# Optimization experiments

Hardware: AMD Instinct MI355X
Metric: run time of the kernel (lower is better)

## Reference

```python
import jax, jax.numpy as jnp
import numpy as np

IMG_H, IMG_W = 900, 1600
NUM_CLASSES = 10
NUM_CAMS = 6

# pcdet boxes_to_corners_3d corner template (unit box, centered)
CORNER_TEMPLATE = jnp.array(
    [[1, 1, -1], [1, -1, -1], [-1, -1, -1], [-1, 1, -1],
     [1, 1, 1], [1, -1, 1], [-1, -1, 1], [-1, 1, 1]], dtype=jnp.float32) * 0.5


def boxes_to_corners_3d(boxes):
    # boxes: [N,7] = (x,y,z,dx,dy,dz,heading) -> [N,8,3]
    dims = boxes[:, 3:6]
    corners = dims[:, None, :] * CORNER_TEMPLATE  # [N,8,3]
    yaw = boxes[:, 6]
    c, s = jnp.cos(yaw), jnp.sin(yaw)
    z = jnp.zeros_like(c)
    o = jnp.ones_like(c)
    # rotate_points_along_z: points @ [[c,s,0],[-s,c,0],[0,0,1]]
    rot = jnp.stack([c, s, z, -s, c, z, z, z, o], axis=-1).reshape(-1, 3, 3)
    corners = jnp.einsum('nkj,njm->nkm', corners, rot)
    return corners + boxes[:, None, 0:3]


def box_iou(a, b):
    # a: [M,4], b: [K,4] xyxy -> [M,K]
    lt = jnp.maximum(a[:, None, :2], b[None, :, :2])
    rb = jnp.minimum(a[:, None, 2:], b[None, :, 2:])
    wh = jnp.clip(rb - lt, 0.0)
    inter = wh[..., 0] * wh[..., 1]
    area_a = (a[:, 2] - a[:, 0]) * (a[:, 3] - a[:, 1])
    area_b = (b[:, 2] - b[:, 0]) * (b[:, 3] - b[:, 1])
    union = area_a[:, None] + area_b[None, :] - inter
    return jnp.where(union > 0, inter / union, 0.0)


def _project_boxes(pred_boxes, img_aug_matrix, lidar_aug_matrix, lidar2image):
    # batch index 0 (B=1); returns proj [6,N,4] and valid [6,N]
    N = pred_boxes.shape[0]
    corners = boxes_to_corners_3d(pred_boxes).reshape(-1, 3)  # [N*8,3]
    la = lidar_aug_matrix[0]
    pts = corners - la[:3, 3]
    pts = jnp.linalg.inv(la[:3, :3]) @ pts.T  # [3, N*8]
    l2i = lidar2image[0]
    cc = l2i[:, :3, :3] @ pts + l2i[:, :3, 3][:, :, None]  # [6,3,N*8]
    zc = jnp.clip(cc[:, 2, :], 1e-5, 1e5)
    xy = cc[:, :2, :] / zc[:, None, :]
    cc = jnp.concatenate([xy, zc[:, None, :]], axis=1)
    ia = img_aug_matrix[0]
    cc = ia[:, :3, :3] @ cc + ia[:, :3, 3][:, :, None]
    pix = jnp.transpose(cc[:, :2, :], (0, 2, 1))  # [6, N*8, 2]
    # .long() truncation (non-differentiable in original)
    pix = jax.lax.stop_gradient(pix).astype(jnp.int32)
    px = jnp.clip(pix[..., 0], 0, IMG_W)
    py = jnp.clip(pix[..., 1], 0, IMG_H)
    pix = jnp.stack([px, py], -1).reshape(NUM_CAMS, N, 8, 2).astype(pred_boxes.dtype)
    xy1 = pix.min(axis=2)  # [6,N,2]
    xy2 = pix.max(axis=2)
    valid = jnp.all((xy2 - xy1) > 0, axis=-1)  # [6,N]
    proj = jnp.concatenate([xy1, xy2], axis=-1)  # [6,N,4]
    return proj, valid


def setup_inputs() -> dict:
    rng = np.random.default_rng(0)
    N, M = 4096, 6144
    xy = rng.uniform(-40, 40, (N, 2))
    zc = rng.uniform(-1, 1, (N, 1))
    dims = rng.uniform(1.0, 4.0, (N, 3))
    yaw = rng.uniform(0, 2 * np.pi, (N, 1))
    pred_boxes = np.concatenate([xy, zc, dims, yaw], axis=1).astype(np.float32)
    # 6 cameras: pinhole intrinsics + yaw-spaced extrinsics
    K = np.array([[1000., 0., 800.], [0., 1000., 450.], [0., 0., 1.]])
    l2i = np.zeros((1, NUM_CAMS, 4, 4), np.float32)
    for ci, ang in enumerate(np.linspace(0, 2 * np.pi, NUM_CAMS, endpoint=False)):
        fwd = np.array([np.cos(ang), np.sin(ang), 0.])
        right = np.array([np.sin(ang), -np.cos(ang), 0.])
        down = np.array([0., 0., -1.])
        R = np.stack([right, down, fwd], 0)
        l2i[0, ci, :3, :3] = K @ R
        l2i[0, ci, 3, 3] = 1.0
    img_aug_matrix = np.tile(np.eye(4, dtype=np.float32), (1, NUM_CAMS, 1, 1))
    lidar_aug_matrix = np.eye(4, dtype=np.float32)[None]
    cx = rng.uniform(0, IMG_W, M)
    cy = rng.uniform(0, IMG_H, M)
    w = rng.uniform(20, 300, M)
    h = rng.uniform(20, 300, M)
    det_boxes = np.stack([np.clip(cx - w / 2, 0, IMG_W), np.clip(cy - h / 2, 0, IMG_H),
                          np.clip(cx + w / 2, 0, IMG_W), np.clip(cy + h / 2, 0, IMG_H)], 1).astype(np.float32)
    det_labels = rng.integers(1, NUM_CLASSES + 1, M).astype(np.int32)
    det_scores = rng.uniform(0.05, 1.0, M).astype(np.float32)
    det_batch_idx = np.zeros(M, np.int32)
    det_cam_idx = (np.arange(M) % NUM_CAMS).astype(np.int32)
    return {
        'pred_boxes': jnp.asarray(pred_boxes),
        'img_aug_matrix': jnp.asarray(img_aug_matrix),
        'lidar_aug_matrix': jnp.asarray(lidar_aug_matrix),
        'lidar2image': jnp.asarray(l2i),
        'det_boxes': jnp.asarray(det_boxes),
        'det_labels': jnp.asarray(det_labels),
        'det_scores': jnp.asarray(det_scores),
        'det_batch_idx': jnp.asarray(det_batch_idx),
        'det_cam_idx': jnp.asarray(det_cam_idx),
    }


def reference(pred_boxes, img_aug_matrix, lidar_aug_matrix, lidar2image,
              det_boxes, det_labels, det_scores, det_batch_idx, det_cam_idx):
    proj, valid = _project_boxes(pred_boxes, img_aug_matrix, lidar_aug_matrix, lidar2image)
    label_matrix = jax.nn.one_hot(det_labels - 1, NUM_CLASSES, dtype=det_scores.dtype) * det_scores[:, None]
    probs_sum = jnp.zeros((pred_boxes.shape[0], NUM_CLASSES), dtype=det_scores.dtype)
    for c in range(NUM_CAMS):
        mask = ((det_cam_idx == c) & (det_batch_idx == 0)).astype(det_boxes.dtype)
        iou = box_iou(det_boxes, proj[c]) * mask[:, None]  # [M,N]
        probs_sum = probs_sum + (iou.T @ label_matrix) * valid[c][:, None]  # [N,10]
    denom = 1e-5 + valid.astype(probs_sum.dtype).sum(axis=0)
    box_probs_mean = probs_sum / denom[:, None]
    pred_scores = jnp.nan_to_num(jnp.max(box_probs_mean, axis=-1), nan=0.0)
    pred_labels = jnp.argmax(box_probs_mean, axis=-1) + 1
    return pred_labels, pred_scores
```

## Files before the change

### kernel.cpp

```cpp
#include <hip/hip_runtime.h>
#include <cstdint>
#include <climits>

#pragma clang fp contract(off)

#define NCAM 6
#define NCLS 10
#define IMGW 1600
#define IMGH 900

__device__ __forceinline__ int sat_f2i(float f) {
    if (f != f) return 0;
    if (f >= 2147483648.0f) return INT_MAX;
    if (f <= -2147483648.0f) return INT_MIN;
    return (int)f;
}

__global__ __launch_bounds__(256) void fused_kernel(
        const float* __restrict__ boxes,
        const float* __restrict__ ia,
        const float* __restrict__ la,
        const float* __restrict__ l2i,
        const float4* __restrict__ det_boxes,
        const int*    __restrict__ det_labels,
        const float*  __restrict__ det_scores,
        const int*    __restrict__ det_batch,
        const int*    __restrict__ det_cam,
        float* __restrict__ out,
        int N, int M) {
    int n = blockIdx.x;
    int tid = threadIdx.x;
    if (n >= N) return;

    __shared__ float sP[NCAM][6];
    __shared__ float red[NCLS][256];

    if (tid < NCAM) {
        int cam = tid;
        float bx = boxes[n*7+0], by = boxes[n*7+1], bz = boxes[n*7+2];
        float dx = boxes[n*7+3], dy = boxes[n*7+4], dz = boxes[n*7+5];
        float yaw = boxes[n*7+6];
        float c = (float)cos((double)yaw);
        float s = (float)sin((double)yaw);

        float a00=la[0],a01=la[1],a02=la[2],t0=la[3];
        float a10=la[4],a11=la[5],a12=la[6],t1=la[7];
        float a20=la[8],a21=la[9],a22=la[10],t2=la[11];
        float det = a00*(a11*a22-a12*a21) - a01*(a10*a22-a12*a20) + a02*(a10*a21-a11*a20);
        float id = 1.0f/det;
        float r00=(a11*a22-a12*a21)*id, r01=(a02*a21-a01*a22)*id, r02=(a01*a12-a02*a11)*id;
        float r10=(a12*a20-a10*a22)*id, r11=(a00*a22-a02*a20)*id, r12=(a02*a10-a00*a12)*id;
        float r20=(a10*a21-a11*a20)*id, r21=(a01*a20-a00*a21)*id, r22=(a00*a11-a01*a10)*id;

        const float* L = l2i + cam*16;
        const float* A = ia  + cam*16;
        int minx = INT_MAX, miny = INT_MAX, maxx = INT_MIN, maxy = INT_MIN;
        #pragma unroll
        for (int k = 0; k < 8; k++) {
            float sx = ((k==0||k==1||k==4||k==5) ?  0.5f : -0.5f) * dx;
            float sy = ((k==0||k==3||k==4||k==7) ?  0.5f : -0.5f) * dy;
            float sz = ((k>=4)                   ?  0.5f : -0.5f) * dz;
            float cx = sx*c - sy*s + bx;
            float cy = sx*s + sy*c + by;
            float cz = sz + bz;
            float ux = cx - t0, uy = cy - t1, uz = cz - t2;
            float PX = r00*ux + r01*uy + r02*uz;
            float PY = r10*ux + r11*uy + r12*uz;
            float PZ = r20*ux + r21*uy + r22*uz;

            float u = L[0]*PX + L[1]*PY + L[2]*PZ  + L[3];
            float v = L[4]*PX + L[5]*PY + L[6]*PZ  + L[7];
            float w = L[8]*PX + L[9]*PY + L[10]*PZ + L[11];
            float zc = fminf(fmaxf(w, 1e-5f), 100000.0f);
            float x = u / zc, y = v / zc;
            float xx = A[0]*x + A[1]*y + A[2]*zc + A[3];
            float yy = A[4]*x + A[5]*y + A[6]*zc + A[7];
            int pxi = sat_f2i(xx); pxi = min(max(pxi, 0), IMGW);
            int pyi = sat_f2i(yy); pyi = min(max(pyi, 0), IMGH);
            minx = min(minx, pxi); maxx = max(maxx, pxi);
            miny = min(miny, pyi); maxy = max(maxy, pyi);
        }
        float x1 = (float)minx, y1 = (float)miny, x2 = (float)maxx, y2 = (float)maxy;
        float validf = ((x2 - x1) > 0.0f && (y2 - y1) > 0.0f) ? 1.0f : 0.0f;
        sP[cam][0] = x1; sP[cam][1] = y1; sP[cam][2] = x2; sP[cam][3] = y2;
        sP[cam][4] = (x2 - x1) * (y2 - y1);
        sP[cam][5] = validf;
    }
    __syncthreads();

    float probs[NCLS];
    #pragma unroll
    for (int k = 0; k < NCLS; k++) probs[k] = 0.0f;

    for (int m = tid; m < M; m += 256) {
        float4 b = det_boxes[m];
        int cam = det_cam[m];
        int bi  = det_batch[m];
        int cls = det_labels[m] - 1;
        float sc = det_scores[m];
        if (bi == 0 && cam >= 0 && cam < NCAM && cls >= 0 && cls < NCLS) {
            const float* P = sP[cam];
            float ltx = fmaxf(b.x, P[0]);
            float lty = fmaxf(b.y, P[1]);
            float rbx = fminf(b.z, P[2]);
            float rby = fminf(b.w, P[3]);
            float iw = fmaxf(rbx - ltx, 0.0f);
            float ih = fmaxf(rby - lty, 0.0f);
            float inter = iw * ih;
            float area_a = (b.z - b.x) * (b.w - b.y);
            float uni = area_a + P[4] - inter;
            float iou = (uni > 0.0f) ? (inter / uni) : 0.0f;
            float w = iou * P[5] * sc;
            #pragma unroll
            for (int k = 0; k < NCLS; k++) probs[k] += (k == cls) ? w : 0.0f;
        }
    }

    #pragma unroll
    for (int k = 0; k < NCLS; k++) red[k][tid] = probs[k];
    __syncthreads();
    for (int s = 128; s > 0; s >>= 1) {
        if (tid < s) {
            #pragma unroll
            for (int k = 0; k < NCLS; k++) red[k][tid] += red[k][tid + s];
        }
        __syncthreads();
    }
    if (tid == 0) {
        float nv = 0.0f;
        for (int c2 = 0; c2 < NCAM; c2++) nv += sP[c2][5];
        float denom = 1e-5f + nv;
        float best = -1.0f; int bestk = 0;
        #pragma unroll
        for (int k = 0; k < NCLS; k++) {
            float v = red[k][0] / denom;
            if (v > best) { best = v; bestk = k; }
        }
        out[n]     = (float)(bestk + 1);
        out[N + n] = best;
    }
}

extern "C" void kernel_launch(void* const* d_in, const int* in_sizes, int n_in,
                              void* d_out, int out_size, void* d_ws, size_t ws_size,
                              hipStream_t stream) {
    const float*  pred_boxes = (const float*)d_in[0];
    const float*  ia         = (const float*)d_in[1];
    const float*  la         = (const float*)d_in[2];
    const float*  l2i        = (const float*)d_in[3];
    const float4* det_boxes  = (const float4*)d_in[4];
    const int*    det_labels = (const int*)d_in[5];
    const float*  det_scores = (const float*)d_in[6];
    const int*    det_batch  = (const int*)d_in[7];
    const int*    det_cam    = (const int*)d_in[8];
    float* out = (float*)d_out;

    int N = in_sizes[0] / 7;
    int M = in_sizes[4] / 4;

    fused_kernel<<<N, 256, 0, stream>>>(pred_boxes, ia, la, l2i,
                                        det_boxes, det_labels, det_scores,
                                        det_batch, det_cam, out, N, M);
}
```

Baseline: 127.4 us.

## Split into sort, projection, chunked IoU and reduce kernels with class-sorted detections

Replaces the single fused kernel, which used one block per predicted box, with a four-kernel pipeline. A single-block kernel bucket-sorts valid detections by (camera, class) and precomputes their areas. A projection kernel assigns one thread per predicted box, and a main kernel assigns one thread per box over detection chunks staged in shared memory. The main kernel walks per-class segments, so it no longer needs the one-hot accumulation or the per-box block reduction, and it switches to fast division. A final kernel sums the chunk partials and takes the argmax. The trade-offs are extra launches and workspace traffic, a serial single-block sort, and fast-division rounding that could alter IoU values.

New measurement: 161.0 us. +26.3%, slower.

```diff
diff --git a/kernel.cpp b/kernel.cpp
--- a/kernel.cpp
+++ b/kernel.cpp
@@ -6,8 +6,10 @@
 
 #define NCAM 6
 #define NCLS 10
+#define NKEY 60
 #define IMGW 1600
 #define IMGH 900
+#define CS_MAX 512
 
 __device__ __forceinline__ int sat_f2i(float f) {
     if (f != f) return 0;
@@ -16,61 +18,117 @@
     return (int)f;
 }
 
-__global__ __launch_bounds__(256) void fused_kernel(
-        const float* __restrict__ boxes,
-        const float* __restrict__ ia,
-        const float* __restrict__ la,
-        const float* __restrict__ l2i,
+__global__ __launch_bounds__(256) void sort_kernel(
         const float4* __restrict__ det_boxes,
         const int*    __restrict__ det_labels,
         const float*  __restrict__ det_scores,
         const int*    __restrict__ det_batch,
         const int*    __restrict__ det_cam,
-        float* __restrict__ out,
-        int N, int M) {
-    int n = blockIdx.x;
-    int tid = threadIdx.x;
+        float*        __restrict__ sdet,
+        int*          __restrict__ seg,
+        unsigned int* __restrict__ keyrank,
+        int M) {
+    __shared__ unsigned int hist[NKEY * 256];
+    __shared__ unsigned int tot[NKEY];
+    __shared__ int kb[NKEY + 1];
+    int t = threadIdx.x;
+    for (int k = t; k < NKEY * 256; k += 256) hist[k] = 0u;
+    __syncthreads();
+
+    int per = (M + 255) >> 8;
+    int b0 = t * per, b1 = min(b0 + per, M);
+    for (int m = b0; m < b1; m++) {
+        int cam = det_cam[m], bi = det_batch[m], cls = det_labels[m] - 1;
+        bool ok = (bi == 0) && (cam >= 0) && (cam < NCAM) && (cls >= 0) && (cls < NCLS);
+        if (ok) {
+            int key = cam * NCLS + cls;
+            unsigned int r = hist[key * 256 + t];
+            hist[key * 256 + t] = r + 1u;
+            keyrank[m] = ((unsigned int)key << 16) | r;
+        } else {
+            keyrank[m] = 0xFFFFFFFFu;
+        }
+    }
+    __syncthreads();
+
+    if (t < NKEY) {
+        unsigned int run = 0;
+        for (int j = 0; j < 256; j++) {
+            unsigned int v = hist[t * 256 + j];
+            hist[t * 256 + j] = run;
+            run += v;
+        }
+        tot[t] = run;
+    }
+    __syncthreads();
+    if (t == 0) {
+        int base = 0;
+        for (int k = 0; k < NKEY; k++) { kb[k] = base; seg[k] = base; base += (int)tot[k]; }
+        kb[NKEY] = base; seg[NKEY] = base;
+    }
+    __syncthreads();
+
+    for (int m = b0; m < b1; m++) {
+        unsigned int v = keyrank[m];
+        if (v == 0xFFFFFFFFu) continue;
+        int key = (int)(v >> 16);
+        int pos = kb[key] + (int)hist[key * 256 + t] + (int)(v & 0xFFFFu);
+        float4 b = det_boxes[m];
+        float area = (b.z - b.x) * (b.w - b.y);
+        float4* o = (float4*)(sdet + (size_t)pos * 8);
+        o[0] = b;
+        o[1] = make_float4(area, det_scores[m], 0.0f, 0.0f);
+    }
+}
+
+__global__ __launch_bounds__(256) void proj_kernel(
+        const float* __restrict__ boxes,
+        const float* __restrict__ ia,
+        const float* __restrict__ la,
+        const float* __restrict__ l2i,
+        float* __restrict__ projW,
+        int N) {
+    int n = blockIdx.x * 256 + threadIdx.x;
     if (n >= N) return;
-
-    __shared__ float sP[NCAM][6];
-    __shared__ float red[NCLS][256];
-
-    if (tid < NCAM) {
-        int cam = tid;
-        float bx = boxes[n*7+0], by = boxes[n*7+1], bz = boxes[n*7+2];
-        float dx = boxes[n*7+3], dy = boxes[n*7+4], dz = boxes[n*7+5];
-        float yaw = boxes[n*7+6];
-        float c = (float)cos((double)yaw);
-        float s = (float)sin((double)yaw);
-
-        float a00=la[0],a01=la[1],a02=la[2],t0=la[3];
-        float a10=la[4],a11=la[5],a12=la[6],t1=la[7];
-        float a20=la[8],a21=la[9],a22=la[10],t2=la[11];
-        float det = a00*(a11*a22-a12*a21) - a01*(a10*a22-a12*a20) + a02*(a10*a21-a11*a20);
-        float id = 1.0f/det;
-        float r00=(a11*a22-a12*a21)*id, r01=(a02*a21-a01*a22)*id, r02=(a01*a12-a02*a11)*id;
-        float r10=(a12*a20-a10*a22)*id, r11=(a00*a22-a02*a20)*id, r12=(a02*a10-a00*a12)*id;
-        float r20=(a10*a21-a11*a20)*id, r21=(a01*a20-a00*a21)*id, r22=(a00*a11-a01*a10)*id;
-
+    float bx = boxes[n*7+0], by = boxes[n*7+1], bz = boxes[n*7+2];
+    float dx = boxes[n*7+3], dy = boxes[n*7+4], dz = boxes[n*7+5];
+    float yaw = boxes[n*7+6];
+    float c = (float)cos((double)yaw);
+    float s = (float)sin((double)yaw);
+
+    float a00=la[0],a01=la[1],a02=la[2],t0=la[3];
+    float a10=la[4],a11=la[5],a12=la[6],t1=la[7];
+    float a20=la[8],a21=la[9],a22=la[10],t2=la[11];
+    float det = a00*(a11*a22-a12*a21) - a01*(a10*a22-a12*a20) + a02*(a10*a21-a11*a20);
+    float id = 1.0f/det;
+    float r00=(a11*a22-a12*a21)*id, r01=(a02*a21-a01*a22)*id, r02=(a01*a12-a02*a11)*id;
+    float r10=(a12*a20-a10*a22)*id, r11=(a00*a22-a02*a20)*id, r12=(a02*a10-a00*a12)*id;
+    float r20=(a10*a21-a11*a20)*id, r21=(a01*a20-a00*a21)*id, r22=(a00*a11-a01*a10)*id;
+
+    float PX[8], PY[8], PZ[8];
+    #pragma unroll
+    for (int k = 0; k < 8; k++) {
+        float sx = ((k==0||k==1||k==4||k==5) ?  0.5f : -0.5f) * dx;
+        float sy = ((k==0||k==3||k==4||k==7) ?  0.5f : -0.5f) * dy;
+        float sz = ((k>=4)                   ?  0.5f : -0.5f) * dz;
+        float cx = sx*c - sy*s + bx;
+        float cy = sx*s + sy*c + by;
+        float cz = sz + bz;
+        float ux = cx - t0, uy = cy - t1, uz = cz - t2;
+        PX[k] = r00*ux + r01*uy + r02*uz;
+        PY[k] = r10*ux + r11*uy + r12*uz;
+        PZ[k] = r20*ux + r21*uy + r22*uz;
+    }
+
+    for (int cam = 0; cam < NCAM; cam++) {
         const float* L = l2i + cam*16;
         const float* A = ia  + cam*16;
         int minx = INT_MAX, miny = INT_MAX, maxx = INT_MIN, maxy = INT_MIN;
         #pragma unroll
         for (int k = 0; k < 8; k++) {
-            float sx = ((k==0||k==1||k==4||k==5) ?  0.5f : -0.5f) * dx;
-            float sy = ((k==0||k==3||k==4||k==7) ?  0.5f : -0.5f) * dy;
-            float sz = ((k>=4)                   ?  0.5f : -0.5f) * dz;
-            float cx = sx*c - sy*s + bx;
-            float cy = sx*s + sy*c + by;
-            float cz = sz + bz;
-            float ux = cx - t0, uy = cy - t1, uz = cz - t2;
-            float PX = r00*ux + r01*uy + r02*uz;
-            float PY = r10*ux + r11*uy + r12*uz;
-            float PZ = r20*ux + r21*uy + r22*uz;
-
-            float u = L[0]*PX + L[1]*PY + L[2]*PZ  + L[3];
-            float v = L[4]*PX + L[5]*PY + L[6]*PZ  + L[7];
-            float w = L[8]*PX + L[9]*PY + L[10]*PZ + L[11];
+            float u = L[0]*PX[k] + L[1]*PY[k] + L[2]*PZ[k]  + L[3];
+            float v = L[4]*PX[k] + L[5]*PY[k] + L[6]*PZ[k]  + L[7];
+            float w = L[8]*PX[k] + L[9]*PY[k] + L[10]*PZ[k] + L[11];
             float zc = fminf(fmaxf(w, 1e-5f), 100000.0f);
             float x = u / zc, y = v / zc;
             float xx = A[0]*x + A[1]*y + A[2]*zc + A[3];
@@ -82,63 +140,105 @@
         }
         float x1 = (float)minx, y1 = (float)miny, x2 = (float)maxx, y2 = (float)maxy;
         float validf = ((x2 - x1) > 0.0f && (y2 - y1) > 0.0f) ? 1.0f : 0.0f;
-        sP[cam][0] = x1; sP[cam][1] = y1; sP[cam][2] = x2; sP[cam][3] = y2;
-        sP[cam][4] = (x2 - x1) * (y2 - y1);
-        sP[cam][5] = validf;
-    }
-    __syncthreads();
-
-    float probs[NCLS];
-    #pragma unroll
-    for (int k = 0; k < NCLS; k++) probs[k] = 0.0f;
-
-    for (int m = tid; m < M; m += 256) {
-        float4 b = det_boxes[m];
-        int cam = det_cam[m];
-        int bi  = det_batch[m];
-        int cls = det_labels[m] - 1;
-        float sc = det_scores[m];
-        if (bi == 0 && cam >= 0 && cam < NCAM && cls >= 0 && cls < NCLS) {
-            const float* P = sP[cam];
-            float ltx = fmaxf(b.x, P[0]);
-            float lty = fmaxf(b.y, P[1]);
-            float rbx = fminf(b.z, P[2]);
-            float rby = fminf(b.w, P[3]);
-            float iw = fmaxf(rbx - ltx, 0.0f);
-            float ih = fmaxf(rby - lty, 0.0f);
-            float inter = iw * ih;
-            float area_a = (b.z - b.x) * (b.w - b.y);
-            float uni = area_a + P[4] - inter;
-            float iou = (uni > 0.0f) ? (inter / uni) : 0.0f;
-            float w = iou * P[5] * sc;
-            #pragma unroll
-            for (int k = 0; k < NCLS; k++) probs[k] += (k == cls) ? w : 0.0f;
-        }
-    }
-
-    #pragma unroll
-    for (int k = 0; k < NCLS; k++) red[k][tid] = probs[k];
-    __syncthreads();
-    for (int s = 128; s > 0; s >>= 1) {
-        if (tid < s) {
-            #pragma unroll
-            for (int k = 0; k < NCLS; k++) red[k][tid] += red[k][tid + s];
-        }
-        __syncthreads();
-    }
-    if (tid == 0) {
-        float nv = 0.0f;
-        for (int c2 = 0; c2 < NCAM; c2++) nv += sP[c2][5];
-        float denom = 1e-5f + nv;
-        float best = -1.0f; int bestk = 0;
+        projW[(cam*6+0)*N + n] = x1;
+        projW[(cam*6+1)*N + n] = y1;
+        projW[(cam*6+2)*N + n] = x2;
+        projW[(cam*6+3)*N + n] = y2;
+        projW[(cam*6+4)*N + n] = (x2 - x1) * (y2 - y1);
+        projW[(cam*6+5)*N + n] = validf;
+    }
+}
+
+__global__ __launch_bounds__(256, 4) void main_kernel(
+        const float* __restrict__ projW,
+        const float* __restrict__ sdet,
+        const int*   __restrict__ seg,
+        float*       __restrict__ partial,
+        int N, int M, int CS) {
+    int tid = threadIdx.x;
+    int box = blockIdx.x * 256 + tid;
+    int chunk = blockIdx.y;
+    int c0 = chunk * CS, c1 = min(c0 + CS, M);
+
+    __shared__ float4 sd[CS_MAX * 2];
+    __shared__ int sseg[NKEY + 1];
+    __shared__ float sprobs[256 * 11];
+
+    int nst = (c1 - c0) * 2;
+    const float4* gsd = (const float4*)sdet;
+    for (int i = tid; i < nst; i += 256) sd[i] = gsd[(size_t)c0 * 2 + i];
+    if (tid <= NKEY) sseg[tid] = seg[tid];
+    #pragma unroll
+    for (int k = 0; k < 11; k++) sprobs[tid * 11 + k] = 0.0f;
+    __syncthreads();
+
+    if (box < N) {
+        for (int cam = 0; cam < NCAM; cam++) {
+            int kb = cam * NCLS;
+            int sA = max(sseg[kb], c0), eA = min(sseg[kb + NCLS], c1);
+            if (sA >= eA) continue;
+            float Px1 = projW[(cam*6+0)*N + box];
+            float Py1 = projW[(cam*6+1)*N + box];
+            float Px2 = projW[(cam*6+2)*N + box];
+            float Py2 = projW[(cam*6+3)*N + box];
+            float Pa  = projW[(cam*6+4)*N + box];
+            float Pv  = projW[(cam*6+5)*N + box];
+            for (int cls = 0; cls < NCLS; cls++) {
+                int s = max(sseg[kb + cls], c0), e = min(sseg[kb + cls + 1], c1);
+                if (s >= e) continue;
+                float acc = 0.0f;
+                const float4* dp = &sd[(s - c0) * 2];
+                for (int m = s; m < e; m++) {
+                    float4 b = dp[0];
+                    float4 q = dp[1];
+                    dp += 2;
+                    float ltx = fmaxf(b.x, Px1);
+                    float lty = fmaxf(b.y, Py1);
+                    float rbx = fminf(b.z, Px2);
+                    float rby = fminf(b.w, Py2);
+                    float iw = fmaxf(rbx - ltx, 0.0f);
+                    float ih = fmaxf(rby - lty, 0.0f);
+                    float inter = iw * ih;
+                    float uni = (q.x + Pa) - inter;
+                    float r = __fdividef(inter, uni);
+                    float iou = (uni > 0.0f) ? r : 0.0f;
+                    acc += iou * q.y;
+                }
+                sprobs[tid * 11 + cls] += acc * Pv;
+            }
+        }
         #pragma unroll
-        for (int k = 0; k < NCLS; k++) {
-            float v = red[k][0] / denom;
-            if (v > best) { best = v; bestk = k; }
-        }
-        out[n]     = (float)(bestk + 1);
-        out[N + n] = best;
-    }
+        for (int k = 0; k < NCLS; k++)
+            partial[((size_t)chunk * NCLS + k) * N + box] = sprobs[tid * 11 + k];
+    }
+}
+
+__global__ __launch_bounds__(256) void reduce_kernel(
+        const float* __restrict__ partial,
+        const float* __restrict__ projW,
+        float* __restrict__ out, int N, int S) {
+    int n = blockIdx.x * 256 + threadIdx.x;
+    if (n >= N) return;
+    float p[NCLS];
+    #pragma unroll
+    for (int k = 0; k < NCLS; k++) p[k] = 0.0f;
+    for (int c = 0; c < S; c++) {
+        #pragma unroll
+        for (int k = 0; k < NCLS; k++)
+            p[k] += partial[((size_t)c * NCLS + k) * N + n];
+    }
+    float nv = 0.0f;
+    #pragma unroll
+    for (int cam = 0; cam < NCAM; cam++) nv += projW[(cam*6+5)*N + n];
+    float denom = 1e-5f + nv;
+    float best = -1e30f; int bk = 0;
+    #pragma unroll
+    for (int k = 0; k < NCLS; k++) {
+        float v = p[k] / denom;
+        if (v > best) { best = v; bk = k; }
+    }
+    out[n]     = (float)(bk + 1);
+    out[N + n] = best;
 }
 
 extern "C" void kernel_launch(void* const* d_in, const int* in_sizes, int n_in,
@@ -158,7 +258,26 @@
     int N = in_sizes[0] / 7;
     int M = in_sizes[4] / 4;
 
-    fused_kernel<<<N, 256, 0, stream>>>(pred_boxes, ia, la, l2i,
-                                        det_boxes, det_labels, det_scores,
-                                        det_batch, det_cam, out, N, M);
-}
+    int S = 32;
+    int CS = (M + S - 1) / S;
+    if (CS > CS_MAX) { S = (M + CS_MAX - 1) / CS_MAX; CS = (M + S - 1) / S; }
+
+    char* w = (char*)d_ws;
+    float*        sdet    = (float*)w;
+    size_t off = (size_t)M * 8 * 4;
+    int*          seg     = (int*)(w + off);
+    off += 256;
+    unsigned int* keyrank = (unsigned int*)(w + off);
+    off += (size_t)M * 4;
+    off = (off + 15) & ~(size_t)15;
+    float*        projW   = (float*)(w + off);
+    off += (size_t)36 * N * 4;
+    float*        partial = (float*)(w + off);
+
+    int gx = (N + 255) / 256;
+    sort_kernel<<<1, 256, 0, stream>>>(det_boxes, det_labels, det_scores,
+                                       det_batch, det_cam, sdet, seg, keyrank, M);
+    proj_kernel<<<gx, 256, 0, stream>>>(pred_boxes, ia, la, l2i, projW, N);
+    main_kernel<<<dim3(gx, S), 256, 0, stream>>>(projW, sdet, seg, partial, N, M, CS);
+    reduce_kernel<<<gx, 256, 0, stream>>>(partial, projW, out, N, S);
+}
```
